# Performance work log

Measured on AMD Instinct MI355X. Metric: run time of the kernel, lower is better.

Reference implementation:

```python
import jax, jax.numpy as jnp
import numpy as np
from jax import lax

EPS_LN = 1e-5
EPS_BN = 1e-5

def layernorm(x, g, b):
    m = x.mean(-1, keepdims=True)
    v = x.var(-1, keepdims=True)
    return (x - m) / jnp.sqrt(v + EPS_LN) * g + b

def conv(x, w, b):
    y = lax.conv_general_dilated(x, w, (1, 1), 'SAME', dimension_numbers=('NCHW', 'OIHW', 'NCHW'))
    return y + b[None, :, None, None]

def bnorm(x, g, b, m, v):
    # BatchNorm2d in eval mode (running stats)
    return (x - m[None, :, None, None]) / jnp.sqrt(v[None, :, None, None] + EPS_BN) * g[None, :, None, None] + b[None, :, None, None]

def maxpool2(x):
    return lax.reduce_window(x, -jnp.inf, lax.max, (1, 1, 2, 2), (1, 1, 2, 2), 'VALID')

def l2norm_rows(x):
    n = jnp.linalg.norm(x, axis=1, keepdims=True)
    return x / jnp.maximum(n, 1e-12)

def fastslow(x, sw, sb, fw, fb, lng, lnb, lr, decay):
    # one hebbian fast-weight update step (torch does this in no_grad on x.detach())
    xs = lax.stop_gradient(x)
    fw = fw * decay
    fb = fb * decay
    slow_out = xs @ sw.T + sb
    xn = l2norm_rows(xs)
    son = l2norm_rows(slow_out)
    hebb = son.T @ xn / xs.shape[0]          # [out,in] outer-product update
    fw = fw + lr * hebb
    wn = jnp.linalg.norm(fw, axis=1, keepdims=True)
    fw = jnp.where(wn > 0.25, fw * (0.25 / (wn + 1e-8)), fw)
    fb = jnp.clip(fb + lr * son.mean(0), -0.2, 0.2)
    fw = lax.stop_gradient(fw)
    fb = lax.stop_gradient(fb)
    out = x @ (sw + fw).T + (sb + fb)
    return layernorm(out, lng, lnb)

def forward(x, c1_w, c1_b, bn1_g, bn1_b, bn1_m, bn1_v,
            c2_w, c2_b, bn2_g, bn2_b, bn2_m, bn2_v,
            c3_w, c3_b, bn3_g, bn3_b, bn3_m, bn3_v,
            core_w, core_b, core_lng, core_lnb,
            fp_sw, fp_sb, fp_fw, fp_fb, fp_lng, fp_lnb,
            sp_sw, sp_sb, sp_fw, sp_fb, sp_lng, sp_lnb,
            int_w, int_b, int_lng, int_lnb, mem,
            cn_w1, cn_b1, cn_lng, cn_lnb, cn_w2, cn_b2,
            pr_w, pr_b, pr_lng, pr_lnb, cl_w, cl_b):
    # encoder (dropout layers are identity in eval)
    h = jax.nn.relu(bnorm(conv(x, c1_w, c1_b), bn1_g, bn1_b, bn1_m, bn1_v)); h = maxpool2(h)
    h = jax.nn.relu(bnorm(conv(h, c2_w, c2_b), bn2_g, bn2_b, bn2_m, bn2_v)); h = maxpool2(h)
    h = jax.nn.relu(bnorm(conv(h, c3_w, c3_b), bn3_g, bn3_b, bn3_m, bn3_v))
    h = h.mean((2, 3))  # AdaptiveAvgPool2d((1,1)) + Flatten -> [B,256]
    # core
    hc = jax.nn.relu(layernorm(h @ core_w.T + core_b, core_lng, core_lnb))
    # dual system: memory EMA (no_grad), fast/slow hebbian paths, integrator
    mem_new = lax.stop_gradient(0.9 * mem + 0.1 * hc.mean(0, keepdims=True))
    fast_out = fastslow(hc, fp_sw, fp_sb, fp_fw, fp_fb, fp_lng, fp_lnb, 0.015, 0.95)
    slow_out = fastslow(hc + 0.3 * mem_new, sp_sw, sp_sb, sp_fw, sp_fb, sp_lng, sp_lnb, 0.005, 0.97)
    comb = jnp.concatenate([fast_out, slow_out], axis=1)
    hd = layernorm(comb @ int_w.T + int_b, int_lng, int_lnb)
    hd = hd + hc  # residual
    # consciousness: phi from eigen-entropy of feature covariance (no_grad)
    a = lax.stop_gradient(hd)
    am = a.mean(0, keepdims=True)
    ast = jnp.std(a, axis=0, keepdims=True, ddof=1) + 1e-6
    an = (a - am) / ast
    n = a.shape[0]
    cov = an.T @ an / (n - 1) + 1e-4 * jnp.eye(a.shape[1], dtype=a.dtype)
    eigs = jnp.clip(jnp.linalg.eigvalsh(cov), 0.0, None)
    en = eigs / (eigs.sum() + 1e-8)
    entropy = -(en * jnp.log(en + 1e-8)).sum()
    phi = entropy / jnp.log(jnp.asarray(float(a.shape[1]), a.dtype))
    phi_eff = jnp.clip(0.3 * phi, 0.0, 1.0)  # running_phi starts at 0: 0.7*0 + 0.3*phi
    net = jax.nn.relu(layernorm(hd @ cn_w1.T + cn_b1, cn_lng, cn_lnb)) @ cn_w2.T + cn_b2
    strength = jax.nn.sigmoid((phi_eff - 0.1) * 5.0)
    coef = jnp.where(phi_eff > 0.1, strength, 0.1)
    hcon = hd + coef * net
    # projection + classifier
    hp = jax.nn.relu(layernorm(hcon @ pr_w.T + pr_b, pr_lng, pr_lnb))
    return hp @ cl_w.T + cl_b

def setup_inputs() -> dict:
    key = jax.random.key(0)
    ks = iter(jax.random.split(key, 64))
    def nrm(shape, s=0.05):
        return jax.random.normal(next(ks), shape, jnp.float32) * s
    B, D = 512, 256
    d = {}
    d['x'] = jax.random.normal(next(ks), (B, 3, 32, 32), jnp.float32)
    for i, (co, ci) in enumerate([(64, 3), (128, 64), (256, 128)], 1):
        d[f'c{i}_w'] = nrm((co, ci, 3, 3))
        d[f'c{i}_b'] = jnp.zeros((co,), jnp.float32)
        d[f'bn{i}_g'] = jnp.ones((co,), jnp.float32)
        d[f'bn{i}_b'] = jnp.zeros((co,), jnp.float32)
        d[f'bn{i}_m'] = jnp.zeros((co,), jnp.float32)
        d[f'bn{i}_v'] = jnp.ones((co,), jnp.float32)
    d['core_w'] = nrm((D, D)); d['core_b'] = jnp.zeros((D,), jnp.float32)
    d['core_lng'] = jnp.ones((D,), jnp.float32); d['core_lnb'] = jnp.zeros((D,), jnp.float32)
    for p in ['fp', 'sp']:
        d[f'{p}_sw'] = nrm((D, D)); d[f'{p}_sb'] = jnp.zeros((D,), jnp.float32)
        d[f'{p}_fw'] = nrm((D, D), 0.01); d[f'{p}_fb'] = jnp.zeros((D,), jnp.float32)
        d[f'{p}_lng'] = jnp.ones((D,), jnp.float32); d[f'{p}_lnb'] = jnp.zeros((D,), jnp.float32)
    d['int_w'] = nrm((D, 2 * D)); d['int_b'] = jnp.zeros((D,), jnp.float32)
    d['int_lng'] = jnp.ones((D,), jnp.float32); d['int_lnb'] = jnp.zeros((D,), jnp.float32)
    d['mem'] = jnp.zeros((1, D), jnp.float32)
    d['cn_w1'] = nrm((D, D)); d['cn_b1'] = jnp.zeros((D,), jnp.float32)
    d['cn_lng'] = jnp.ones((D,), jnp.float32); d['cn_lnb'] = jnp.zeros((D,), jnp.float32)
    d['cn_w2'] = nrm((D, D)); d['cn_b2'] = jnp.zeros((D,), jnp.float32)
    d['pr_w'] = nrm((128, D)); d['pr_b'] = jnp.zeros((128,), jnp.float32)
    d['pr_lng'] = jnp.ones((128,), jnp.float32); d['pr_lnb'] = jnp.zeros((128,), jnp.float32)
    d['cl_w'] = nrm((10, 128)); d['cl_b'] = jnp.zeros((10,), jnp.float32)
    return d

def reference(x, c1_w, c1_b, bn1_g, bn1_b, bn1_m, bn1_v,
              c2_w, c2_b, bn2_g, bn2_b, bn2_m, bn2_v,
              c3_w, c3_b, bn3_g, bn3_b, bn3_m, bn3_v,
              core_w, core_b, core_lng, core_lnb,
              fp_sw, fp_sb, fp_fw, fp_fb, fp_lng, fp_lnb,
              sp_sw, sp_sb, sp_fw, sp_fb, sp_lng, sp_lnb,
              int_w, int_b, int_lng, int_lnb, mem,
              cn_w1, cn_b1, cn_lng, cn_lnb, cn_w2, cn_b2,
              pr_w, pr_b, pr_lng, pr_lnb, cl_w, cl_b):
    return forward(x, c1_w, c1_b, bn1_g, bn1_b, bn1_m, bn1_v,
                   c2_w, c2_b, bn2_g, bn2_b, bn2_m, bn2_v,
                   c3_w, c3_b, bn3_g, bn3_b, bn3_m, bn3_v,
                   core_w, core_b, core_lng, core_lnb,
                   fp_sw, fp_sb, fp_fw, fp_fb, fp_lng, fp_lnb,
                   sp_sw, sp_sb, sp_fw, sp_fb, sp_lng, sp_lnb,
                   int_w, int_b, int_lng, int_lnb, mem,
                   cn_w1, cn_b1, cn_lng, cn_lnb, cn_w2, cn_b2,
                   pr_w, pr_b, pr_lng, pr_lnb, cl_w, cl_b)
```

## Files before the change

### kernel.cpp

```cpp
#include <hip/hip_runtime.h>
#include <hip/hip_bf16.h>

template<int NT>
__device__ __forceinline__ float block_sum(float v, float* red, int t) {
  red[t] = v; __syncthreads();
#pragma unroll
  for (int s = NT/2; s > 0; s >>= 1) {
    if (t < s) red[t] += red[t+s];
    __syncthreads();
  }
  float r = red[0];
  __syncthreads();
  return r;
}

template<int DIN>
__device__ __forceinline__ float dot_f32_row(const float* __restrict__ wr, const float* __restrict__ xs) {
  float acc = 0.f;
  const float4* wp = reinterpret_cast<const float4*>(wr);
#pragma unroll 4
  for (int i = 0; i < DIN/4; ++i) {
    float4 w4 = wp[i];
    acc += w4.x*xs[i*4] + w4.y*xs[i*4+1] + w4.z*xs[i*4+2] + w4.w*xs[i*4+3];
  }
  return acc;
}

__global__ __launch_bounds__(256) void k_conv1(const float* __restrict__ x, const float* __restrict__ w1,
    const float* __restrict__ cb, const float* __restrict__ g, const float* __restrict__ bb,
    const float* __restrict__ m, const float* __restrict__ v, float* __restrict__ p1)
{
  __shared__ float xs[3][34][34];
  __shared__ float ws1[64*27];
  __shared__ float A1[64], B1[64];
  int b = blockIdx.x, t = threadIdx.x;
  float* xsf = &xs[0][0][0];
  for (int i = t; i < 3*34*34; i += 256) xsf[i] = 0.f;
  for (int i = t; i < 64*27; i += 256) ws1[i] = w1[i];
  if (t < 64) {
    float sc = g[t] * rsqrtf(v[t] + 1e-5f);
    A1[t] = sc;
    B1[t] = (cb[t] - m[t])*sc + bb[t];
  }
  __syncthreads();
  for (int i = t; i < 3*1024; i += 256) {
    int ci = i >> 10, rem = i & 1023, y = rem >> 5, xx = rem & 31;
    xs[ci][y+1][xx+1] = x[((size_t)b*3 + ci)*1024 + rem];
  }
  __syncthreads();
  int py = t >> 4, px = t & 15;
  int y0 = py*2, x0 = px*2;
  for (int co = 0; co < 64; ++co) {
    float a00=0.f,a01=0.f,a10=0.f,a11=0.f;
#pragma unroll
    for (int ci = 0; ci < 3; ++ci) {
      const float* xb = &xs[ci][y0][x0];
      float r0a=xb[0],r0b=xb[1],r0c=xb[2],r0d=xb[3];
      float r1a=xb[34],r1b=xb[35],r1c=xb[36],r1d=xb[37];
      float r2a=xb[68],r2b=xb[69],r2c=xb[70],r2d=xb[71];
      float r3a=xb[102],r3b=xb[103],r3c=xb[104],r3d=xb[105];
      const float* wp = &ws1[co*27 + ci*9];
      float ww0=wp[0],ww1=wp[1],ww2=wp[2],ww3=wp[3],ww4=wp[4],ww5=wp[5],ww6=wp[6],ww7=wp[7],ww8=wp[8];
      a00 += ww0*r0a+ww1*r0b+ww2*r0c + ww3*r1a+ww4*r1b+ww5*r1c + ww6*r2a+ww7*r2b+ww8*r2c;
      a01 += ww0*r0b+ww1*r0c+ww2*r0d + ww3*r1b+ww4*r1c+ww5*r1d + ww6*r2b+ww7*r2c+ww8*r2d;
      a10 += ww0*r1a+ww1*r1b+ww2*r1c + ww3*r2a+ww4*r2b+ww5*r2c + ww6*r3a+ww7*r3b+ww8*r3c;
      a11 += ww0*r1b+ww1*r1c+ww2*r1d + ww3*r2b+ww4*r2c+ww5*r2d + ww6*r3b+ww7*r3c+ww8*r3d;
    }
    float sc = A1[co], sh = B1[co];
    float vmax = fmaxf(fmaxf(a00*sc+sh, a01*sc+sh), fmaxf(a10*sc+sh, a11*sc+sh));
    vmax = fmaxf(vmax, 0.f);
    p1[(((size_t)b*64 + co)*16 + py)*16 + px] = vmax;
  }
}

__global__ __launch_bounds__(256) void k_conv2(const float* __restrict__ p1, const float* __restrict__ w2,
    const float* __restrict__ cb, const float* __restrict__ g, const float* __restrict__ bb,
    const float* __restrict__ m, const float* __restrict__ v, float* __restrict__ p2)
{
  __shared__ float xs[64][18][18];
  __shared__ float wchT[576*5];
  __shared__ float A2[128], B2[128];
  int b = blockIdx.x, t = threadIdx.x;
  float* xsf = &xs[0][0][0];
  for (int i = t; i < 64*18*18; i += 256) xsf[i] = 0.f;
  if (t < 128) {
    float sc = g[t] * rsqrtf(v[t] + 1e-5f);
    A2[t] = sc;
    B2[t] = (cb[t] - m[t])*sc + bb[t];
  }
  __syncthreads();
  for (int i = t; i < 64*256; i += 256) {
    int ci = i >> 8, rem = i & 255, y = rem >> 4, xx = rem & 15;
    xs[ci][y+1][xx+1] = p1[((size_t)b*64 + ci)*256 + rem];
  }
  int lane = t & 3, pos = t >> 2;
  int py = pos >> 3, px = pos & 7;
  int y0 = py*2, x0 = px*2;
  for (int it = 0; it < 32; ++it) {
    __syncthreads();
    for (int i = t; i < 2304; i += 256) {
      int rem = i % 576, co = i / 576;
      wchT[rem*5 + co] = w2[(size_t)it*2304 + i];
    }
    __syncthreads();
    float a00=0.f,a01=0.f,a10=0.f,a11=0.f;
    for (int ci = 0; ci < 64; ++ci) {
      const float* xb = &xs[ci][y0][x0];
      float r0a=xb[0],r0b=xb[1],r0c=xb[2],r0d=xb[3];
      float r1a=xb[18],r1b=xb[19],r1c=xb[20],r1d=xb[21];
      float r2a=xb[36],r2b=xb[37],r2c=xb[38],r2d=xb[39];
      float r3a=xb[54],r3b=xb[55],r3c=xb[56],r3d=xb[57];
      const float* wp = &wchT[(ci*9)*5 + lane];
      float ww0=wp[0],ww1=wp[5],ww2=wp[10],ww3=wp[15],ww4=wp[20],ww5=wp[25],ww6=wp[30],ww7=wp[35],ww8=wp[40];
      a00 += ww0*r0a+ww1*r0b+ww2*r0c + ww3*r1a+ww4*r1b+ww5*r1c + ww6*r2a+ww7*r2b+ww8*r2c;
      a01 += ww0*r0b+ww1*r0c+ww2*r0d + ww3*r1b+ww4*r1c+ww5*r1d + ww6*r2b+ww7*r2c+ww8*r2d;
      a10 += ww0*r1a+ww1*r1b+ww2*r1c + ww3*r2a+ww4*r2b+ww5*r2c + ww6*r3a+ww7*r3b+ww8*r3c;
      a11 += ww0*r1b+ww1*r1c+ww2*r1d + ww3*r2b+ww4*r2c+ww5*r2d + ww6*r3b+ww7*r3c+ww8*r3d;
    }
    int co = it*4 + lane;
    float sc = A2[co], sh = B2[co];
    float vmax = fmaxf(fmaxf(a00*sc+sh, a01*sc+sh), fmaxf(a10*sc+sh, a11*sc+sh));
    vmax = fmaxf(vmax, 0.f);
    p2[(((size_t)b*128 + co)*8 + py)*8 + px] = vmax;
  }
}

__global__ __launch_bounds__(256) void k_conv3(const float* __restrict__ p2, const float* __restrict__ w3,
    const float* __restrict__ cb, const float* __restrict__ g, const float* __restrict__ bb,
    const float* __restrict__ m, const float* __restrict__ v, float* __restrict__ h)
{
  __shared__ float xs[128][10][10];
  __shared__ float wchT[1152*17];
  __shared__ float A3[256], B3[256];
  __shared__ float red2[256];
  int b = blockIdx.x, t = threadIdx.x;
  float* xsf = &xs[0][0][0];
  for (int i = t; i < 128*100; i += 256) xsf[i] = 0.f;
  {
    float sc = g[t] * rsqrtf(v[t] + 1e-5f);
    A3[t] = sc;
    B3[t] = (cb[t] - m[t])*sc + bb[t];
  }
  __syncthreads();
  for (int i = t; i < 128*64; i += 256) {
    int ci = i >> 6, rem = i & 63, y = rem >> 3, xx = rem & 7;
    xs[ci][y+1][xx+1] = p2[((size_t)b*128 + ci)*64 + rem];
  }
  int lane = t & 15, cluster = t >> 4;
  int cy = cluster >> 2, cx = cluster & 3;
  int y0 = cy*2, x0 = cx*2;
  for (int it = 0; it < 16; ++it) {
    __syncthreads();
    for (int i = t; i < 18432; i += 256) {
      int rem = i % 1152, co = i / 1152;
      wchT[rem*17 + co] = w3[(size_t)it*18432 + i];
    }
    __syncthreads();
    float a00=0.f,a01=0.f,a10=0.f,a11=0.f;
    for (int ci = 0; ci < 128; ++ci) {
      const float* xb = &xs[ci][y0][x0];
      float r0a=xb[0],r0b=xb[1],r0c=xb[2],r0d=xb[3];
      float r1a=xb[10],r1b=xb[11],r1c=xb[12],r1d=xb[13];
      float r2a=xb[20],r2b=xb[21],r2c=xb[22],r2d=xb[23];
      float r3a=xb[30],r3b=xb[31],r3c=xb[32],r3d=xb[33];
      const float* wp = &wchT[(ci*9)*17 + lane];
      float ww0=wp[0],ww1=wp[17],ww2=wp[34],ww3=wp[51],ww4=wp[68],ww5=wp[85],ww6=wp[102],ww7=wp[119],ww8=wp[136];
      a00 += ww0*r0a+ww1*r0b+ww2*r0c + ww3*r1a+ww4*r1b+ww5*r1c + ww6*r2a+ww7*r2b+ww8*r2c;
      a01 += ww0*r0b+ww1*r0c+ww2*r0d + ww3*r1b+ww4*r1c+ww5*r1d + ww6*r2b+ww7*r2c+ww8*r2d;
      a10 += ww0*r1a+ww1*r1b+ww2*r1c + ww3*r2a+ww4*r2b+ww5*r2c + ww6*r3a+ww7*r3b+ww8*r3c;
      a11 += ww0*r1b+ww1*r1c+ww2*r1d + ww3*r2b+ww4*r2c+ww5*r2d + ww6*r3b+ww7*r3c+ww8*r3d;
    }
    int co = it*16 + lane;
    float sc = A3[co], sh = B3[co];
    float local = fmaxf(a00*sc+sh,0.f)+fmaxf(a01*sc+sh,0.f)+fmaxf(a10*sc+sh,0.f)+fmaxf(a11*sc+sh,0.f);
    red2[cluster*16 + lane] = local;
    __syncthreads();
    if (t < 16) {
      float s2 = 0.f;
      for (int c2 = 0; c2 < 16; ++c2) s2 += red2[c2*16 + t];
      h[(size_t)b*256 + it*16 + t] = s2 * (1.f/64.f);
    }
  }
}

template<int DIN, int DOUT, bool RELU, bool RESID>
__global__ __launch_bounds__(DOUT) void k_lin_ln(
    const float* __restrict__ in, const float* __restrict__ W, const float* __restrict__ bias,
    const float* __restrict__ g, const float* __restrict__ be,
    const float* __restrict__ resid, float* __restrict__ out, int ostride, int ooff)
{
  __shared__ float xs[DIN];
  __shared__ float red[DOUT];
  int b = blockIdx.x, t = threadIdx.x;
  for (int i = t; i < DIN; i += DOUT) xs[i] = in[(size_t)b*DIN + i];
  __syncthreads();
  float acc = dot_f32_row<DIN>(W + (size_t)t*DIN, xs) + bias[t];
  float mean = block_sum<DOUT>(acc, red, t) * (1.f/DOUT);
  float dv = acc - mean;
  float var = block_sum<DOUT>(dv*dv, red, t) * (1.f/DOUT);
  float y = dv * rsqrtf(var + 1e-5f) * g[t] + be[t];
  if (RELU) y = fmaxf(y, 0.f);
  if (RESID) y += resid[(size_t)b*DOUT + t];
  out[(size_t)b*ostride + ooff + t] = y;
}

__global__ __launch_bounds__(256) void k_lin_rownorm(const float* __restrict__ in, const float* __restrict__ sw,
    const float* __restrict__ sb, float* __restrict__ sout, float* __restrict__ xninv, float* __restrict__ sninv)
{
  int b = blockIdx.x, t = threadIdx.x;
  __shared__ float xs[256];
  __shared__ float red[256];
  xs[t] = in[(size_t)b*256 + t];
  __syncthreads();
  float acc = dot_f32_row<256>(sw + (size_t)t*256, xs) + sb[t];
  sout[(size_t)b*256 + t] = acc;
  float xn2 = block_sum<256>(xs[t]*xs[t], red, t);
  float sn2 = block_sum<256>(acc*acc, red, t);
  if (t == 0) {
    xninv[b] = 1.f / fmaxf(sqrtf(xn2), 1e-12f);
    sninv[b] = 1.f / fmaxf(sqrtf(sn2), 1e-12f);
  }
}

__global__ __launch_bounds__(256) void k_hebb(const float* __restrict__ x, const float* __restrict__ s,
    const float* __restrict__ xninv, const float* __restrict__ sninv,
    const float* __restrict__ sw, const float* __restrict__ fw,
    const float* __restrict__ sb, const float* __restrict__ fb,
    float lr, float decay, float* __restrict__ weff, float* __restrict__ beff)
{
  int o = blockIdx.x, t = threadIdx.x;
  __shared__ float c[512];
  __shared__ float sonb[512];
  __shared__ float red[256];
  for (int b = t; b < 512; b += 256) {
    float son = s[(size_t)b*256 + o] * sninv[b];
    sonb[b] = son;
    c[b] = son * xninv[b];
  }
  __syncthreads();
  float acc = 0.f;
  for (int b = 0; b < 512; ++b) acc += c[b] * x[(size_t)b*256 + t];
  float hebb = acc * (1.f/512.f);
  float fwn = fw[(size_t)o*256 + t] * decay + lr * hebb;
  float wn2 = block_sum<256>(fwn*fwn, red, t);
  float wn = sqrtf(wn2);
  float scale = (wn > 0.25f) ? 0.25f/(wn + 1e-8f) : 1.f;
  weff[(size_t)o*256 + t] = sw[(size_t)o*256 + t] + fwn*scale;
  float sm = block_sum<256>(sonb[t] + sonb[t+256], red, t) * (1.f/512.f);
  if (t == 0) {
    float fbe = fb[o] * decay + lr * sm;
    fbe = fminf(fmaxf(fbe, -0.2f), 0.2f);
    beff[o] = sb[o] + fbe;
  }
}

__global__ __launch_bounds__(256) void k_mem(const float* __restrict__ hc, const float* __restrict__ mem,
                                             float* __restrict__ memnew)
{
  int t = threadIdx.x;
  float s = 0.f;
  for (int b = 0; b < 512; ++b) s += hc[(size_t)b*256 + t];
  memnew[t] = 0.9f*mem[t] + 0.1f*(s * (1.f/512.f));
}

__global__ __launch_bounds__(256) void k_x2(const float* __restrict__ hc, const float* __restrict__ memnew,
                                            float* __restrict__ x2)
{
  int i = blockIdx.x*256 + threadIdx.x;
  x2[i] = hc[i] + 0.3f*memnew[i & 255];
}

__global__ __launch_bounds__(256) void k_colstats(const float* __restrict__ hd, float* __restrict__ am,
                                                  float* __restrict__ ainv)
{
  int t = threadIdx.x;
  float s1 = 0.f;
  for (int b = 0; b < 512; ++b) s1 += hd[(size_t)b*256 + t];
  float mean = s1 * (1.f/512.f);
  float s2 = 0.f;
  for (int b = 0; b < 512; ++b) { float dv = hd[(size_t)b*256 + t] - mean; s2 += dv*dv; }
  am[t] = mean;
  ainv[t] = 1.f/(sqrtf(s2 * (1.f/511.f)) + 1e-6f);
}

__global__ __launch_bounds__(256) void k_cov(const float* __restrict__ hd, const float* __restrict__ am,
    const float* __restrict__ ainv, float* __restrict__ cov)
{
  int i = blockIdx.x, t = threadIdx.x;
  __shared__ float ci[512];
  float ami = am[i], aii = ainv[i];
  for (int b = t; b < 512; b += 256) ci[b] = (hd[(size_t)b*256 + i] - ami)*aii;
  __syncthreads();
  float amj = am[t], aij = ainv[t];
  float acc = 0.f;
  for (int b = 0; b < 512; ++b) acc += ci[b] * (hd[(size_t)b*256 + t] - amj);
  float cval = acc * aij * (1.f/511.f) + ((i == t) ? 1e-4f : 0.f);
  cov[(size_t)i*256 + t] = cval;
}

__global__ __launch_bounds__(1024) void k_tridiag(const float* __restrict__ A, float* __restrict__ d, float* __restrict__ e)
{
  const int n = 256;
  __shared__ float tri[32896];
  __shared__ float v[256], q[256];
  __shared__ float ppw[16][257];
  __shared__ float redA[4], red4[4];
  __shared__ float sH;
  int t = threadIdx.x;
  int wid = t >> 6, lane = t & 63;

  for (int i = t; i < 32896; i += 1024) {
    int r = (int)((sqrtf(8.f*(float)i + 1.f) - 1.f) * 0.5f);
    while ((r+1)*(r+2)/2 <= i) ++r;
    while (r*(r+1)/2 > i) --r;
    int c = i - r*(r+1)/2;
    tri[i] = A[(size_t)r*n + c];
  }
  __syncthreads();

  for (int k = 0; k < n-2; ++k) {
    int m = n-1-k;
    int base = k+1;

    float xi = 0.f;
    if (t < m) {
      int R = base + t;
      xi = tri[R*(R+1)/2 + k];
      v[t] = xi;
    }
    if (t < 256) {
      float val = xi*xi;
#pragma unroll
      for (int mk = 1; mk < 64; mk <<= 1) val += __shfl_xor(val, mk, 64);
      if (lane == 0) redA[wid] = val;
    }
    __syncthreads();
    if (t == 0) {
      float sigma = redA[0]+redA[1]+redA[2]+redA[3];
      float x0 = v[0];
      float alpha = (x0 >= 0.f) ? -sqrtf(sigma) : sqrtf(sigma);
      sH = sigma - x0*alpha;
      e[k] = alpha;
      v[0] = x0 - alpha;
    }
    __syncthreads();
    float H = sH;
    if (H <= 1e-32f) continue;

    float p0=0.f, p1=0.f, p2=0.f, p3=0.f;
    for (int r = wid; r < m; r += 16) {
      int R = base + r;
      int rowoff = R*(R+1)/2 + base;
      float vr = v[r];
      float dot = 0.f;
#pragma unroll
      for (int c = 0; c < 4; ++c) {
        if (64*c <= r) {
          int j = 64*c + lane;
          float val = (j <= r) ? tri[rowoff + j] : 0.f;
          dot += val * v[j];
          float sval = (j < r) ? val : 0.f;
          float contrib = sval * vr;
          if (c == 0) p0 += contrib; else if (c == 1) p1 += contrib;
          else if (c == 2) p2 += contrib; else p3 += contrib;
        }
      }
#pragma unroll
      for (int mk = 1; mk < 64; mk <<= 1) dot += __shfl_xor(dot, mk, 64);
      if (lane == (r & 63)) {
        int sl = r >> 6;
        if (sl == 0) p0 += dot; else if (sl == 1) p1 += dot;
        else if (sl == 2) p2 += dot; else p3 += dot;
      }
    }
    ppw[wid][lane]      = p0;
    ppw[wid][64+lane]   = p1;
    ppw[wid][128+lane]  = p2;
    ppw[wid][192+lane]  = p3;
    __syncthreads();

    float pt = 0.f;
    if (t < 256) {
      float kv = 0.f;
#pragma unroll
      for (int w2 = 0; w2 < 16; ++w2) pt += ppw[w2][t];
      pt /= H;
      if (t < m) kv = v[t] * pt;
#pragma unroll
      for (int mk = 1; mk < 64; mk <<= 1) kv += __shfl_xor(kv, mk, 64);
      if (lane == 0) red4[wid] = kv;
    }
    __syncthreads();
    if (t < m) {
      float Kv = (red4[0]+red4[1]+red4[2]+red4[3]) / (2.f*H);
      q[t] = pt - Kv*v[t];
    }
    __syncthreads();

    for (int r = wid; r < m; r += 16) {
      int R = base + r;
      int rowoff = R*(R+1)/2 + base;
      float vr = v[r], qr = q[r];
#pragma unroll
      for (int c = 0; c < 4; ++c) {
        if (64*c <= r) {
          int j = 64*c + lane;
          if (j <= r) tri[rowoff + j] -= vr*q[j] + qr*v[j];
        }
      }
    }
    __syncthreads();
  }
  if (t == 0) {
    e[n-2] = tri[((n-1)*n)/2 + (n-2)];
    e[n-1] = 0.f;
  }
  if (t < n) d[t] = tri[(t*(t+1))/2 + t];
}

__global__ __launch_bounds__(256) void k_eig_coef(const float* __restrict__ dg, const float* __restrict__ eg,
                                                  float* __restrict__ coefout)
{
  const int n = 256;
  int t = threadIdx.x;
  __shared__ float sd[256], se2[256], sea[256], red[256];
  sd[t] = dg[t];
  float ev = (t < n-1) ? eg[t] : 0.f;
  se2[t] = ev*ev;
  sea[t] = fabsf(ev);
  __syncthreads();
  float r = ((t > 0) ? sea[t-1] : 0.f) + sea[t];
  red[t] = sd[t] - r; __syncthreads();
  for (int s = 128; s > 0; s >>= 1) { if (t < s) red[t] = fminf(red[t], red[t+s]); __syncthreads(); }
  float glo = red[0] - 1e-3f; __syncthreads();
  red[t] = sd[t] + r; __syncthreads();
  for (int s = 128; s > 0; s >>= 1) { if (t < s) red[t] = fmaxf(red[t], red[t+s]); __syncthreads(); }
  float ghi = red[0] + 1e-3f; __syncthreads();

  float lo = glo, hi = ghi;
  for (int it = 0; it < 28; ++it) {
    float mid = 0.5f*(lo + hi);
    int cnt = 0;
    float qq = sd[0] - mid;
    cnt += (qq < 0.f);
    for (int i = 1; i < n; ++i) {
      float denom = qq;
      if (fabsf(denom) < 1e-20f) denom = (denom < 0.f) ? -1e-20f : 1e-20f;
      qq = sd[i] - mid - se2[i-1]/denom;
      cnt += (qq < 0.f);
    }
    if (cnt <= t) lo = mid; else hi = mid;
  }
  float lam = fmaxf(0.5f*(lo + hi), 0.f);
  float tot = block_sum<256>(lam, red, t) + 1e-8f;
  float en = lam / tot;
  float contrib = -en * logf(en + 1e-8f);
  float ent = block_sum<256>(contrib, red, t);
  if (t == 0) {
    float phi = ent / logf(256.f);
    float phi_eff = fminf(fmaxf(0.3f*phi, 0.f), 1.f);
    float strength = 1.f/(1.f + expf(-(phi_eff - 0.1f)*5.f));
    coefout[0] = (phi_eff > 0.1f) ? strength : 0.1f;
  }
}

__global__ __launch_bounds__(256) void k_cn(const float* __restrict__ hd, const float* __restrict__ W1,
    const float* __restrict__ b1, const float* __restrict__ g, const float* __restrict__ be,
    const float* __restrict__ W2, const float* __restrict__ b2, const float* __restrict__ coefp,
    float* __restrict__ hcon)
{
  __shared__ float xs[256];
  __shared__ float t1s[256];
  __shared__ float red[256];
  int b = blockIdx.x, t = threadIdx.x;
  xs[t] = hd[(size_t)b*256 + t];
  __syncthreads();
  float acc = dot_f32_row<256>(W1 + (size_t)t*256, xs) + b1[t];
  float mean = block_sum<256>(acc, red, t) * (1.f/256.f);
  float dv = acc - mean;
  float var = block_sum<256>(dv*dv, red, t) * (1.f/256.f);
  t1s[t] = fmaxf(dv * rsqrtf(var + 1e-5f) * g[t] + be[t], 0.f);
  __syncthreads();
  float acc2 = dot_f32_row<256>(W2 + (size_t)t*256, t1s) + b2[t];
  hcon[(size_t)b*256 + t] = xs[t] + coefp[0]*acc2;
}

__global__ __launch_bounds__(128) void k_pr_cls(const float* __restrict__ hcon, const float* __restrict__ W,
    const float* __restrict__ bias, const float* __restrict__ g, const float* __restrict__ be,
    const float* __restrict__ Wc, const float* __restrict__ bc, float* __restrict__ out)
{
  __shared__ float xs[256];
  __shared__ float hp[128];
  __shared__ float red[128];
  int b = blockIdx.x, t = threadIdx.x;
  xs[t] = hcon[(size_t)b*256 + t];
  xs[t+128] = hcon[(size_t)b*256 + t + 128];
  __syncthreads();
  float acc = dot_f32_row<256>(W + (size_t)t*256, xs) + bias[t];
  float mean = block_sum<128>(acc, red, t) * (1.f/128.f);
  float dv = acc - mean;
  float var = block_sum<128>(dv*dv, red, t) * (1.f/128.f);
  hp[t] = fmaxf(dv * rsqrtf(var + 1e-5f) * g[t] + be[t], 0.f);
  __syncthreads();
  if (t < 10) {
    float a2 = bc[t];
    const float* wr = Wc + (size_t)t*128;
    for (int i = 0; i < 128; ++i) a2 += wr[i]*hp[i];
    out[(size_t)b*10 + t] = a2;
  }
}

extern "C" void kernel_launch(void* const* d_in, const int* in_sizes, int n_in,
                              void* d_out, int out_size, void* d_ws, size_t ws_size,
                              hipStream_t stream)
{
  (void)in_sizes; (void)n_in; (void)out_size; (void)ws_size;
  const float* x     = (const float*)d_in[0];
  const float* c1w   = (const float*)d_in[1];
  const float* c1b   = (const float*)d_in[2];
  const float* bn1g  = (const float*)d_in[3];
  const float* bn1b  = (const float*)d_in[4];
  const float* bn1m  = (const float*)d_in[5];
  const float* bn1v  = (const float*)d_in[6];
  const float* c2w   = (const float*)d_in[7];
  const float* c2b   = (const float*)d_in[8];
  const float* bn2g  = (const float*)d_in[9];
  const float* bn2b  = (const float*)d_in[10];
  const float* bn2m  = (const float*)d_in[11];
  const float* bn2v  = (const float*)d_in[12];
  const float* c3w   = (const float*)d_in[13];
  const float* c3b   = (const float*)d_in[14];
  const float* bn3g  = (const float*)d_in[15];
  const float* bn3b  = (const float*)d_in[16];
  const float* bn3m  = (const float*)d_in[17];
  const float* bn3v  = (const float*)d_in[18];
  const float* corew = (const float*)d_in[19];
  const float* coreb = (const float*)d_in[20];
  const float* corelng = (const float*)d_in[21];
  const float* corelnb = (const float*)d_in[22];
  const float* fpsw  = (const float*)d_in[23];
  const float* fpsb  = (const float*)d_in[24];
  const float* fpfw  = (const float*)d_in[25];
  const float* fpfb  = (const float*)d_in[26];
  const float* fplng = (const float*)d_in[27];
  const float* fplnb = (const float*)d_in[28];
  const float* spsw  = (const float*)d_in[29];
  const float* spsb  = (const float*)d_in[30];
  const float* spfw  = (const float*)d_in[31];
  const float* spfb  = (const float*)d_in[32];
  const float* splng = (const float*)d_in[33];
  const float* splnb = (const float*)d_in[34];
  const float* intw  = (const float*)d_in[35];
  const float* intb  = (const float*)d_in[36];
  const float* intlng= (const float*)d_in[37];
  const float* intlnb= (const float*)d_in[38];
  const float* memi  = (const float*)d_in[39];
  const float* cnw1  = (const float*)d_in[40];
  const float* cnb1  = (const float*)d_in[41];
  const float* cnlng = (const float*)d_in[42];
  const float* cnlnb = (const float*)d_in[43];
  const float* cnw2  = (const float*)d_in[44];
  const float* cnb2  = (const float*)d_in[45];
  const float* prw   = (const float*)d_in[46];
  const float* prb   = (const float*)d_in[47];
  const float* prlng = (const float*)d_in[48];
  const float* prlnb = (const float*)d_in[49];
  const float* clw   = (const float*)d_in[50];
  const float* clb   = (const float*)d_in[51];
  float* out = (float*)d_out;

  float* w = (float*)d_ws;
  size_t off = 0;
  auto alloc = [&](size_t nel) { float* p = w + off; off += nel; return p; };
  float* p1     = alloc((size_t)512*64*16*16);
  float* p2     = alloc((size_t)512*128*8*8);
  float* h      = alloc(512*256);
  float* hc     = alloc(512*256);
  float* x2     = alloc(512*256);
  float* s      = alloc(512*256);
  float* xninv  = alloc(512);
  float* sninv  = alloc(512);
  float* memnew = alloc(256);
  float* weff   = alloc(256*256);
  float* beff   = alloc(256);
  float* comb   = alloc((size_t)512*512);
  float* hd     = alloc(512*256);
  float* am     = alloc(256);
  float* ainv   = alloc(256);
  float* cov    = alloc(256*256);
  float* dvec   = alloc(256);
  float* evec   = alloc(256);
  float* coefb  = alloc(8);
  float* hcon   = alloc(512*256);

  k_conv1<<<512,256,0,stream>>>(x, c1w, c1b, bn1g, bn1b, bn1m, bn1v, p1);
  k_conv2<<<512,256,0,stream>>>(p1, c2w, c2b, bn2g, bn2b, bn2m, bn2v, p2);
  k_conv3<<<512,256,0,stream>>>(p2, c3w, c3b, bn3g, bn3b, bn3m, bn3v, h);
  k_lin_ln<256,256,true,false><<<512,256,0,stream>>>(h, corew, coreb, corelng, corelnb, nullptr, hc, 256, 0);
  k_mem<<<1,256,0,stream>>>(hc, memi, memnew);
  k_x2<<<512,256,0,stream>>>(hc, memnew, x2);
  k_lin_rownorm<<<512,256,0,stream>>>(hc, fpsw, fpsb, s, xninv, sninv);
  k_hebb<<<256,256,0,stream>>>(hc, s, xninv, sninv, fpsw, fpfw, fpsb, fpfb, 0.015f, 0.95f, weff, beff);
  k_lin_ln<256,256,false,false><<<512,256,0,stream>>>(hc, weff, beff, fplng, fplnb, nullptr, comb, 512, 0);
  k_lin_rownorm<<<512,256,0,stream>>>(x2, spsw, spsb, s, xninv, sninv);
  k_hebb<<<256,256,0,stream>>>(x2, s, xninv, sninv, spsw, spfw, spsb, spfb, 0.005f, 0.97f, weff, beff);
  k_lin_ln<256,256,false,false><<<512,256,0,stream>>>(x2, weff, beff, splng, splnb, nullptr, comb, 512, 256);
  k_lin_ln<512,256,false,true><<<512,256,0,stream>>>(comb, intw, intb, intlng, intlnb, hc, hd, 256, 0);
  k_colstats<<<1,256,0,stream>>>(hd, am, ainv);
  k_cov<<<256,256,0,stream>>>(hd, am, ainv, cov);
  k_tridiag<<<1,1024,0,stream>>>(cov, dvec, evec);
  k_eig_coef<<<1,256,0,stream>>>(dvec, evec, coefb);
  k_cn<<<512,256,0,stream>>>(hd, cnw1, cnb1, cnlng, cnlnb, cnw2, cnb2, coefb, hcon);
  k_pr_cls<<<512,128,0,stream>>>(hcon, prw, prb, prlng, prlnb, clw, clb, out);
}
```

Before: 4.009 ms.

## Read conv weights directly from global and parallelize column reductions

Result: slower. 4.625 ms (+15.4%).

```diff
diff --git a/kernel.cpp b/kernel.cpp
--- a/kernel.cpp
+++ b/kernel.cpp
@@ -78,7 +78,6 @@
     const float* __restrict__ m, const float* __restrict__ v, float* __restrict__ p2)
 {
   __shared__ float xs[64][18][18];
-  __shared__ float wchT[576*5];
   __shared__ float A2[128], B2[128];
   int b = blockIdx.x, t = threadIdx.x;
   float* xsf = &xs[0][0][0];
@@ -93,16 +92,13 @@
     int ci = i >> 8, rem = i & 255, y = rem >> 4, xx = rem & 15;
     xs[ci][y+1][xx+1] = p1[((size_t)b*64 + ci)*256 + rem];
   }
+  __syncthreads();
   int lane = t & 3, pos = t >> 2;
   int py = pos >> 3, px = pos & 7;
   int y0 = py*2, x0 = px*2;
   for (int it = 0; it < 32; ++it) {
-    __syncthreads();
-    for (int i = t; i < 2304; i += 256) {
-      int rem = i % 576, co = i / 576;
-      wchT[rem*5 + co] = w2[(size_t)it*2304 + i];
-    }
-    __syncthreads();
+    int co = it*4 + lane;
+    const float* wco = w2 + (size_t)co*576;
     float a00=0.f,a01=0.f,a10=0.f,a11=0.f;
     for (int ci = 0; ci < 64; ++ci) {
       const float* xb = &xs[ci][y0][x0];
@@ -110,14 +106,13 @@
       float r1a=xb[18],r1b=xb[19],r1c=xb[20],r1d=xb[21];
       float r2a=xb[36],r2b=xb[37],r2c=xb[38],r2d=xb[39];
       float r3a=xb[54],r3b=xb[55],r3c=xb[56],r3d=xb[57];
-      const float* wp = &wchT[(ci*9)*5 + lane];
-      float ww0=wp[0],ww1=wp[5],ww2=wp[10],ww3=wp[15],ww4=wp[20],ww5=wp[25],ww6=wp[30],ww7=wp[35],ww8=wp[40];
+      const float* wp = wco + ci*9;
+      float ww0=wp[0],ww1=wp[1],ww2=wp[2],ww3=wp[3],ww4=wp[4],ww5=wp[5],ww6=wp[6],ww7=wp[7],ww8=wp[8];
       a00 += ww0*r0a+ww1*r0b+ww2*r0c + ww3*r1a+ww4*r1b+ww5*r1c + ww6*r2a+ww7*r2b+ww8*r2c;
       a01 += ww0*r0b+ww1*r0c+ww2*r0d + ww3*r1b+ww4*r1c+ww5*r1d + ww6*r2b+ww7*r2c+ww8*r2d;
       a10 += ww0*r1a+ww1*r1b+ww2*r1c + ww3*r2a+ww4*r2b+ww5*r2c + ww6*r3a+ww7*r3b+ww8*r3c;
       a11 += ww0*r1b+ww1*r1c+ww2*r1d + ww3*r2b+ww4*r2c+ww5*r2d + ww6*r3b+ww7*r3c+ww8*r3d;
     }
-    int co = it*4 + lane;
     float sc = A2[co], sh = B2[co];
     float vmax = fmaxf(fmaxf(a00*sc+sh, a01*sc+sh), fmaxf(a10*sc+sh, a11*sc+sh));
     vmax = fmaxf(vmax, 0.f);
@@ -130,7 +125,6 @@
     const float* __restrict__ m, const float* __restrict__ v, float* __restrict__ h)
 {
   __shared__ float xs[128][10][10];
-  __shared__ float wchT[1152*17];
   __shared__ float A3[256], B3[256];
   __shared__ float red2[256];
   int b = blockIdx.x, t = threadIdx.x;
@@ -146,16 +140,13 @@
     int ci = i >> 6, rem = i & 63, y = rem >> 3, xx = rem & 7;
     xs[ci][y+1][xx+1] = p2[((size_t)b*128 + ci)*64 + rem];
   }
+  __syncthreads();
   int lane = t & 15, cluster = t >> 4;
   int cy = cluster >> 2, cx = cluster & 3;
   int y0 = cy*2, x0 = cx*2;
   for (int it = 0; it < 16; ++it) {
-    __syncthreads();
-    for (int i = t; i < 18432; i += 256) {
-      int rem = i % 1152, co = i / 1152;
-      wchT[rem*17 + co] = w3[(size_t)it*18432 + i];
-    }
-    __syncthreads();
+    int co = it*16 + lane;
+    const float* wco = w3 + (size_t)co*1152;
     float a00=0.f,a01=0.f,a10=0.f,a11=0.f;
     for (int ci = 0; ci < 128; ++ci) {
       const float* xb = &xs[ci][y0][x0];
@@ -163,14 +154,13 @@
       float r1a=xb[10],r1b=xb[11],r1c=xb[12],r1d=xb[13];
       float r2a=xb[20],r2b=xb[21],r2c=xb[22],r2d=xb[23];
       float r3a=xb[30],r3b=xb[31],r3c=xb[32],r3d=xb[33];
-      const float* wp = &wchT[(ci*9)*17 + lane];
-      float ww0=wp[0],ww1=wp[17],ww2=wp[34],ww3=wp[51],ww4=wp[68],ww5=wp[85],ww6=wp[102],ww7=wp[119],ww8=wp[136];
+      const float* wp = wco + ci*9;
+      float ww0=wp[0],ww1=wp[1],ww2=wp[2],ww3=wp[3],ww4=wp[4],ww5=wp[5],ww6=wp[6],ww7=wp[7],ww8=wp[8];
       a00 += ww0*r0a+ww1*r0b+ww2*r0c + ww3*r1a+ww4*r1b+ww5*r1c + ww6*r2a+ww7*r2b+ww8*r2c;
       a01 += ww0*r0b+ww1*r0c+ww2*r0d + ww3*r1b+ww4*r1c+ww5*r1d + ww6*r2b+ww7*r2c+ww8*r2d;
       a10 += ww0*r1a+ww1*r1b+ww2*r1c + ww3*r2a+ww4*r2b+ww5*r2c + ww6*r3a+ww7*r3b+ww8*r3c;
       a11 += ww0*r1b+ww1*r1c+ww2*r1d + ww3*r2b+ww4*r2c+ww5*r2d + ww6*r3b+ww7*r3c+ww8*r3d;
     }
-    int co = it*16 + lane;
     float sc = A3[co], sh = B3[co];
     float local = fmaxf(a00*sc+sh,0.f)+fmaxf(a01*sc+sh,0.f)+fmaxf(a10*sc+sh,0.f)+fmaxf(a11*sc+sh,0.f);
     red2[cluster*16 + lane] = local;
@@ -180,6 +170,7 @@
       for (int c2 = 0; c2 < 16; ++c2) s2 += red2[c2*16 + t];
       h[(size_t)b*256 + it*16 + t] = s2 * (1.f/64.f);
     }
+    __syncthreads();
   }
 }
 
@@ -254,12 +245,29 @@
   }
 }
 
-__global__ __launch_bounds__(256) void k_mem(const float* __restrict__ hc, const float* __restrict__ mem,
-                                             float* __restrict__ memnew)
+__global__ __launch_bounds__(256) void k_colpart(const float* __restrict__ src,
+    float* __restrict__ psum, float* __restrict__ psumsq)
+{
+  int j = blockIdx.x, t = threadIdx.x;
+  float s1 = 0.f, s2 = 0.f;
+#pragma unroll
+  for (int r = 0; r < 8; ++r) {
+    float val = src[((size_t)j*8 + r)*256 + t];
+    s1 += val;
+    s2 += val*val;
+  }
+  psum[t*64 + j] = s1;
+  psumsq[t*64 + j] = s2;
+}
+
+__global__ __launch_bounds__(256) void k_mem_fin(const float* __restrict__ psum, const float* __restrict__ mem,
+                                                 float* __restrict__ memnew)
 {
   int t = threadIdx.x;
   float s = 0.f;
-  for (int b = 0; b < 512; ++b) s += hc[(size_t)b*256 + t];
+  const float* p = psum + t*64;
+#pragma unroll 8
+  for (int j = 0; j < 64; ++j) s += p[j];
   memnew[t] = 0.9f*mem[t] + 0.1f*(s * (1.f/512.f));
 }
 
@@ -270,17 +278,19 @@
   x2[i] = hc[i] + 0.3f*memnew[i & 255];
 }
 
-__global__ __launch_bounds__(256) void k_colstats(const float* __restrict__ hd, float* __restrict__ am,
-                                                  float* __restrict__ ainv)
+__global__ __launch_bounds__(256) void k_colstats_fin(const float* __restrict__ psum, const float* __restrict__ psumsq,
+                                                       float* __restrict__ am, float* __restrict__ ainv)
 {
   int t = threadIdx.x;
-  float s1 = 0.f;
-  for (int b = 0; b < 512; ++b) s1 += hd[(size_t)b*256 + t];
+  float s1 = 0.f, s2 = 0.f;
+  const float* p1 = psum + t*64;
+  const float* p2 = psumsq + t*64;
+#pragma unroll 8
+  for (int j = 0; j < 64; ++j) { s1 += p1[j]; s2 += p2[j]; }
   float mean = s1 * (1.f/512.f);
-  float s2 = 0.f;
-  for (int b = 0; b < 512; ++b) { float dv = hd[(size_t)b*256 + t] - mean; s2 += dv*dv; }
+  float var = fmaxf((s2 - 512.f*mean*mean) * (1.f/511.f), 0.f);
   am[t] = mean;
-  ainv[t] = 1.f/(sqrtf(s2 * (1.f/511.f)) + 1e-6f);
+  ainv[t] = 1.f/(sqrtf(var) + 1e-6f);
 }
 
 __global__ __launch_bounds__(256) void k_cov(const float* __restrict__ hd, const float* __restrict__ am,
@@ -592,12 +602,15 @@
   float* evec   = alloc(256);
   float* coefb  = alloc(8);
   float* hcon   = alloc(512*256);
+  float* psum   = alloc(256*64);
+  float* psumsq = alloc(256*64);
 
   k_conv1<<<512,256,0,stream>>>(x, c1w, c1b, bn1g, bn1b, bn1m, bn1v, p1);
   k_conv2<<<512,256,0,stream>>>(p1, c2w, c2b, bn2g, bn2b, bn2m, bn2v, p2);
   k_conv3<<<512,256,0,stream>>>(p2, c3w, c3b, bn3g, bn3b, bn3m, bn3v, h);
   k_lin_ln<256,256,true,false><<<512,256,0,stream>>>(h, corew, coreb, corelng, corelnb, nullptr, hc, 256, 0);
-  k_mem<<<1,256,0,stream>>>(hc, memi, memnew);
+  k_colpart<<<64,256,0,stream>>>(hc, psum, psumsq);
+  k_mem_fin<<<1,256,0,stream>>>(psum, memi, memnew);
   k_x2<<<512,256,0,stream>>>(hc, memnew, x2);
   k_lin_rownorm<<<512,256,0,stream>>>(hc, fpsw, fpsb, s, xninv, sninv);
   k_hebb<<<256,256,0,stream>>>(hc, s, xninv, sninv, fpsw, fpfw, fpsb, fpfb, 0.015f, 0.95f, weff, beff);
@@ -606,7 +619,8 @@
   k_hebb<<<256,256,0,stream>>>(x2, s, xninv, sninv, spsw, spfw, spsb, spfb, 0.005f, 0.97f, weff, beff);
   k_lin_ln<256,256,false,false><<<512,256,0,stream>>>(x2, weff, beff, splng, splnb, nullptr, comb, 512, 256);
   k_lin_ln<512,256,false,true><<<512,256,0,stream>>>(comb, intw, intb, intlng, intlnb, hc, hd, 256, 0);
-  k_colstats<<<1,256,0,stream>>>(hd, am, ainv);
+  k_colpart<<<64,256,0,stream>>>(hd, psum, psumsq);
+  k_colstats_fin<<<1,256,0,stream>>>(psum, psumsq, am, ainv);
   k_cov<<<256,256,0,stream>>>(hd, am, ainv, cov);
   k_tridiag<<<1,1024,0,stream>>>(cov, dvec, evec);
   k_eig_coef<<<1,256,0,stream>>>(dvec, evec, coefb);
```
